# Performance work log

Measured on AMD Instinct MI355X. Metric: run time of the kernel, lower is better.

## Reference

```python
import jax, jax.numpy as jnp
import numpy as np

DIM = 512
HEADS = 8
DIM_HEAD = 64
DIM_INNER = HEADS * DIM_HEAD
SCALE = DIM_HEAD ** -0.5


def setup_inputs() -> dict:
    key = jax.random.key(0)
    ks = jax.random.split(key, 8)
    b, n = 2, 1024
    x = jax.random.normal(ks[0], (b, n, DIM), dtype=jnp.float32)
    w = lambda k, i, o: jax.random.normal(k, (i, o), dtype=jnp.float32) * 0.02
    return {
        'x': x,
        'w_q_u': w(ks[1], DIM, DIM_INNER),
        'w_k_u': w(ks[2], DIM, DIM_INNER),
        'w_v_u': w(ks[3], DIM, DIM_INNER),
        'w_q_c': w(ks[4], DIM, DIM_INNER),
        'w_k_c': w(ks[5], DIM, DIM_INNER),
        'w_v_c': w(ks[6], DIM, DIM_INNER),
        'w_out': w(ks[7], DIM_INNER, DIM),
    }


def reference(x, w_q_u, w_k_u, w_v_u, w_q_c, w_k_c, w_v_c, w_out):
    b, n, _ = x.shape

    def proj(w):  # [b,n,dim] -> [b,h,n,d]
        return (x @ w).reshape(b, n, HEADS, DIM_HEAD).transpose(0, 2, 1, 3)

    q_u, k_u, v_u = proj(w_q_u), proj(w_k_u), proj(w_v_u)
    q_c, k_c, v_c = proj(w_q_c), proj(w_k_c), proj(w_v_c)

    idx = jnp.arange(n)
    causal = idx[:, None] >= idx[None, :]  # tril ones (binary causal mask)

    # term1 = (q_c @ v_u^T) * scale, zeroed above diagonal
    term1 = jnp.einsum('bhid,bhjd->bhij', q_c, v_u) * SCALE
    term1 = term1 * causal.astype(term1.dtype)

    # sigmoid term: (q_u @ k_u^T)*scale with lookahead mask tril(-inf, diag=0)
    logits_u = jnp.einsum('bhid,bhjd->bhij', q_u, k_u) * SCALE
    sig = jax.nn.sigmoid(jnp.where(causal, -jnp.inf, logits_u))

    # S_u[i,k] = sum_j term1[i,j] * sig[k,j]
    S_u = jnp.einsum('bhij,bhkj->bhik', term1, sig)

    # S_c: causal-masked QK
    S_c = jnp.einsum('bhid,bhjd->bhij', q_c, k_c) * SCALE
    S_c = jnp.where(causal, S_c, -jnp.inf)

    final_scores = S_c - jax.nn.silu(S_u)
    attn = jax.nn.softmax(final_scores, axis=-1)
    out = jnp.einsum('bhij,bhjd->bhid', attn, v_c)  # [b,h,n,d]
    out = out.transpose(0, 2, 1, 3).reshape(b, n, DIM_INNER)
    return out @ w_out
```

## Files before the change

kernel.cpp:

```cpp
#include <hip/hip_runtime.h>
#include <math.h>


typedef __bf16 bf16x8 __attribute__((ext_vector_type(8)));
typedef float f32x4 __attribute__((ext_vector_type(4)));

#define SCALE 0.125f

#define GLL(g, l) __builtin_amdgcn_global_load_lds(                         \
    (const __attribute__((address_space(1))) void*)(g),                     \
    (__attribute__((address_space(3))) void*)(l), 16, 0, 0)

__device__ __forceinline__ unsigned short f2bf(float f){
  unsigned int x = __builtin_bit_cast(unsigned int, f);
  unsigned int r = (x + 0x7fffu + ((x >> 16) & 1u)) >> 16;
  return (unsigned short)r;
}
__device__ __forceinline__ float bf2f(unsigned short u){
  unsigned int x = ((unsigned int)u) << 16;
  return __builtin_bit_cast(float, x);
}
__device__ __forceinline__ f32x4 mfma16(bf16x8 a, bf16x8 b, f32x4 c){
  return __builtin_amdgcn_mfma_f32_16x16x32_bf16(a, b, c, 0, 0, 0);
}
__device__ __forceinline__ bf16x8 ld8(const unsigned short* p){
  return *(const bf16x8*)p;
}

__device__ const unsigned char QK_CUM[16] =
  {0,1,2,4,6,9,12,16,20,25,30,36,42,49,56,64};

__device__ const unsigned char FL_RB[40] =
  {15,14,13,12,15,11,14,10,13, 9,12, 8,15,11, 7,14,10, 6,13, 9,
    5,12, 8, 4,15,11, 7, 3,14,10, 6, 2,13, 9, 5, 1,12, 8, 4, 0};
__device__ const unsigned char FL_G[40] =
  { 0, 0, 0, 0, 1, 0, 1, 0, 1, 0, 1, 0, 2, 1, 0, 2, 1, 0, 2, 1,
    0, 2, 1, 0, 3, 2, 1, 0, 3, 2, 1, 0, 3, 2, 1, 0, 3, 2, 1, 0};

__global__ __launch_bounds__(256) void k_prep(
    const float* __restrict__ x,
    const float* __restrict__ w0, const float* __restrict__ w1,
    const float* __restrict__ w2, const float* __restrict__ w3,
    const float* __restrict__ w4, const float* __restrict__ w5,
    const float* __restrict__ w6,
    unsigned short* __restrict__ xb, unsigned short* __restrict__ wT){
  int t = threadIdx.x;
  if (blockIdx.x < 576){
    for (int i = blockIdx.x * 256 + t; i < 262144; i += 576 * 256){
      float4 v = ((const float4*)x)[i];
      ushort4 o; o.x = f2bf(v.x); o.y = f2bf(v.y); o.z = f2bf(v.z); o.w = f2bf(v.w);
      ((ushort4*)xb)[i] = o;
    }
    return;
  }
  __shared__ float lds[64 * 65];
  int bx = blockIdx.x - 576;
  int mat = bx >> 6, tile = bx & 63, tr = tile >> 3, tc = tile & 7;
  int k0 = tr * 64, c0 = tc * 64;
  const float* src;
  switch (mat){
    case 0: src = w0; break; case 1: src = w1; break; case 2: src = w2; break;
    case 3: src = w3; break; case 4: src = w4; break; case 5: src = w5; break;
    default: src = w6; break;
  }
#pragma unroll
  for (int i = 0; i < 4; ++i){
    int r = (t >> 4) + i * 16, c4 = (t & 15) * 4;
    float4 v = *(const float4*)(src + (size_t)(k0 + r) * 512 + c0 + c4);
    lds[r * 65 + c4 + 0] = v.x; lds[r * 65 + c4 + 1] = v.y;
    lds[r * 65 + c4 + 2] = v.z; lds[r * 65 + c4 + 3] = v.w;
  }
  __syncthreads();
  unsigned short* dst = wT + (size_t)mat * 262144;
#pragma unroll
  for (int i = 0; i < 4; ++i){
    int oc = (t >> 4) + i * 16;
    int kq = (t & 15) * 4;
    ushort4 o;
    o.x = f2bf(lds[(kq + 0) * 65 + oc]);
    o.y = f2bf(lds[(kq + 1) * 65 + oc]);
    o.z = f2bf(lds[(kq + 2) * 65 + oc]);
    o.w = f2bf(lds[(kq + 3) * 65 + oc]);
    *(ushort4*)(dst + (size_t)(c0 + oc) * 512 + k0 + kq) = o;
  }
}

__global__ __launch_bounds__(256) void k_proj(
    const unsigned short* __restrict__ xb, const unsigned short* __restrict__ wT,
    unsigned short* __restrict__ P){
  __shared__ __align__(16) unsigned short sA[2 * 2 * 64 * 32];
  __shared__ __align__(16) unsigned short sB[2 * 2 * 128 * 32];
  int t = threadIdx.x, lane = t & 63, l16 = lane & 15, quad = lane >> 4;
  int w = t >> 6, wm = w >> 1, wn = w & 1;
  int bx = blockIdx.x;
  int mt = bx / 24, nt = bx - mt * 24;
  int M0 = mt * 64, N0 = nt * 128;
  int matb = N0 >> 9;
  int nin = N0 & 511;
  int srow = (lane >> 2), scol = (lane & 3) * 8;
  const unsigned short* gA = xb + (size_t)(M0 + w*16 + srow) * 512 + scol;
  const unsigned short* gB = wT + (size_t)matb * 262144
                               + (size_t)(nin + w*32 + srow) * 512 + scol;
  unsigned short* lA = sA + (w*16) * 32;
  unsigned short* lB = sB + (w*32) * 32;
  f32x4 acc[4][2] = {};
#define STAGE_PROJ(buf, k0) do {                                   \
    GLL(gA + (k0),               lA + (buf)*4096);                 \
    GLL(gB + (k0),               lB + (buf)*8192);                 \
    GLL(gB + (k0) + 16*512,      lB + (buf)*8192 + 16*32);         \
    GLL(gA + (k0) + 32,          lA + (buf)*4096 + 2048);          \
    GLL(gB + (k0) + 32,          lB + (buf)*8192 + 4096);          \
    GLL(gB + (k0) + 32 + 16*512, lB + (buf)*8192 + 4096 + 16*32);  \
  } while(0)
  STAGE_PROJ(0, 0);
  for (int it = 0; it < 8; ++it){
    if (it < 7){
      STAGE_PROJ((it+1) & 1, (it+1)*64);
      asm volatile("s_waitcnt vmcnt(6)" ::: "memory");
    } else {
      asm volatile("s_waitcnt vmcnt(0)" ::: "memory");
    }
    __builtin_amdgcn_s_barrier();
    int b = it & 1;
#pragma unroll
    for (int h = 0; h < 2; ++h){
      bf16x8 aw[4], ax[2];
#pragma unroll
      for (int fi = 0; fi < 4; ++fi)
        aw[fi] = *(const bf16x8*)(sB + b*8192 + h*4096 + (wn*64 + fi*16 + l16) * 32 + quad * 8);
#pragma unroll
      for (int mi = 0; mi < 2; ++mi)
        ax[mi] = *(const bf16x8*)(sA + b*4096 + h*2048 + (wm*32 + mi*16 + l16) * 32 + quad * 8);
#pragma unroll
      for (int fi = 0; fi < 4; ++fi)
#pragma unroll
        for (int mi = 0; mi < 2; ++mi)
          acc[fi][mi] = mfma16(aw[fi], ax[mi], acc[fi][mi]);
    }
    __builtin_amdgcn_s_barrier();
  }
#undef STAGE_PROJ
#pragma unroll
  for (int fi = 0; fi < 4; ++fi)
#pragma unroll
    for (int mi = 0; mi < 2; ++mi){
      int row = M0 + wm*32 + mi*16 + l16;
      int b_ = row >> 10, n_ = row & 1023;
      int c0 = N0 + wn*64 + fi*16 + quad*4;
      int h = (c0 & 511) >> 6, d = c0 & 63;
      int bh = b_*8 + h;
      ushort4 o;
      o.x = f2bf(acc[fi][mi][0]); o.y = f2bf(acc[fi][mi][1]);
      o.z = f2bf(acc[fi][mi][2]); o.w = f2bf(acc[fi][mi][3]);
      *(ushort4*)(P + (size_t)(matb*16 + bh) * 65536 + (size_t)n_ * 64 + d) = o;
    }
}

__global__ __launch_bounds__(256) void k_qk_vct(
    const unsigned short* __restrict__ P,
    unsigned short* __restrict__ term1, unsigned short* __restrict__ sig,
    unsigned short* __restrict__ vcT){
  int t = threadIdx.x;
  if (blockIdx.x < 256){
    __shared__ unsigned short lds[64 * 72];
    int bh = blockIdx.x >> 4, nt = blockIdx.x & 15;
    int N0 = nt * 64;
    const unsigned short* src = P + (size_t)(5*16 + bh) * 65536 + (size_t)N0 * 64;
#pragma unroll
    for (int i2 = 0; i2 < 2; ++i2){
      int id = i2 * 256 + t;
      int r = id >> 3, c8 = (id & 7) * 8;
      ushort4 v0 = *(const ushort4*)(src + r * 64 + c8);
      ushort4 v1 = *(const ushort4*)(src + r * 64 + c8 + 4);
      *(ushort4*)(lds + r * 72 + c8) = v0;
      *(ushort4*)(lds + r * 72 + c8 + 4) = v1;
    }
    __syncthreads();
    unsigned short* dst = vcT + (size_t)bh * 65536;
#pragma unroll
    for (int i2 = 0; i2 < 2; ++i2){
      int id = i2 * 256 + t;
      int dd = id >> 3, n8 = (id & 7) * 8;
      ushort4 a, b;
      a.x = lds[(n8+0)*72 + dd]; a.y = lds[(n8+1)*72 + dd];
      a.z = lds[(n8+2)*72 + dd]; a.w = lds[(n8+3)*72 + dd];
      b.x = lds[(n8+4)*72 + dd]; b.y = lds[(n8+5)*72 + dd];
      b.z = lds[(n8+6)*72 + dd]; b.w = lds[(n8+7)*72 + dd];
      *(ushort4*)(dst + (size_t)dd * 1024 + N0 + n8) = a;
      *(ushort4*)(dst + (size_t)dd * 1024 + N0 + n8 + 4) = b;
    }
    return;
  }
  __shared__ unsigned short sA[2 * 64 * 32], sB[2 * 128 * 32];
  int id = blockIdx.x - 256;
  int bh = id & 15, tt = id >> 4;
  int mat = (tt >= 72);
  int tl = mat ? tt - 72 : tt;
  int rb = 15;
  while (QK_CUM[rb] > tl) --rb;
  int ct = tl - QK_CUM[rb];
  int R0, C0;
  const unsigned short *Asrc, *Bsrc;
  if (!mat){ R0 = rb * 64;        C0 = ct * 128;
             Asrc = P + (size_t)(3*16 + bh) * 65536;
             Bsrc = P + (size_t)(2*16 + bh) * 65536; }
  else     { R0 = (15 - rb) * 64; C0 = (7 - ct) * 128;
             Asrc = P + (size_t)(0*16 + bh) * 65536;
             Bsrc = P + (size_t)(1*16 + bh) * 65536; }
  int lane = t & 63, l16 = lane & 15, quad = lane >> 4;
  int w = t >> 6, wm = w >> 1, wn = w & 1;
  int srow = lane >> 2, scol = (lane & 3) * 8;
  const unsigned short* gA = Asrc + (size_t)(R0 + w*16 + srow) * 64 + scol;
  const unsigned short* gB = Bsrc + (size_t)(C0 + w*32 + srow) * 64 + scol;
  unsigned short* lA0 = sA + (w*16) * 32;
  unsigned short* lB0 = sB + (w*32) * 32;
  unsigned short* lA1 = lA0 + 64 * 32;
  unsigned short* lB1 = lB0 + 128 * 32;
  f32x4 acc[4][2] = {};
  GLL(gA,              lA0);
  GLL(gB,              lB0);
  GLL(gB + 16*64,      lB0 + 16*32);
  GLL(gA + 32,         lA1);
  GLL(gB + 32,         lB1);
  GLL(gB + 32 + 16*64, lB1 + 16*32);
  __syncthreads();
#pragma unroll
  for (int h = 0; h < 2; ++h){
    bf16x8 af[2], bfr[4];
#pragma unroll
    for (int mi = 0; mi < 2; ++mi)
      af[mi] = *(const bf16x8*)(sA + h*2048 + (wm*32 + mi*16 + l16) * 32 + quad * 8);
#pragma unroll
    for (int fi = 0; fi < 4; ++fi)
      bfr[fi] = *(const bf16x8*)(sB + h*4096 + (wn*64 + fi*16 + l16) * 32 + quad * 8);
#pragma unroll
    for (int fi = 0; fi < 4; ++fi)
#pragma unroll
      for (int mi = 0; mi < 2; ++mi)
        acc[fi][mi] = mfma16(bfr[fi], af[mi], acc[fi][mi]);
  }
  unsigned short* out = (mat ? sig : term1) + (size_t)bh * 1048576;
#pragma unroll
  for (int fi = 0; fi < 4; ++fi)
#pragma unroll
    for (int mi = 0; mi < 2; ++mi){
      int row = R0 + wm*32 + mi*16 + l16;
      int c0 = C0 + wn*64 + fi*16 + quad*4;
      ushort4 o;
#pragma unroll
      for (int r = 0; r < 4; ++r){
        int col = c0 + r;
        float v = acc[fi][mi][r] * SCALE;
        unsigned short res;
        if (!mat) res = (col <= row) ? f2bf(v) : (unsigned short)0;
        else      res = (col >  row) ? f2bf(1.f / (1.f + expf(-v))) : (unsigned short)0;
        ((unsigned short*)&o)[r] = res;
      }
      *(ushort4*)(out + (size_t)row * 1024 + c0) = o;
    }
}

__global__ __launch_bounds__(256) void k_flash(
    const unsigned short* __restrict__ P,
    const unsigned short* __restrict__ term1,
    const unsigned short* __restrict__ sig,
    const unsigned short* __restrict__ vcT,
    float* __restrict__ Opart, float* __restrict__ MS,
    unsigned short* __restrict__ O2){
  __shared__ __align__(16) unsigned short sA[2 * 64 * 32];
  __shared__ __align__(16) unsigned short sB[2 * 128 * 32];
  __shared__ __align__(16) unsigned short probs[64 * 136];
  __shared__ float wpm[2][64], wps[2][64];
  __shared__ float alpha_s[64], mrun_s[64], srun_s[64];
  int t = threadIdx.x;
  int bh = blockIdx.x & 15, q = blockIdx.x >> 4;
  int rb = FL_RB[q], g = FL_G[q];
  int T = (rb >> 1) + 1, G = (T + 1) >> 1;
  int ct0 = 2 * g, ctN = min(ct0 + 2, T);
  int R0 = rb * 64;
  size_t sbase = (size_t)bh * 1048576;
  int lane = t & 63, l16 = lane & 15, quad = lane >> 4, w = t >> 6;
  int wm = w >> 1, wn = w & 1;
  int srow = lane >> 2, scol = (lane & 3) * 8;
  unsigned short* lA0 = sA + (w*16) * 32;
  unsigned short* lB0 = sB + (w*32) * 32;
  unsigned short* lA1 = lA0 + 2048;
  unsigned short* lB1 = lB0 + 4096;
  const unsigned short* Qc = P + (size_t)(3*16 + bh) * 65536;
  const unsigned short* Kc = P + (size_t)(4*16 + bh) * 65536;
  const unsigned short* Vt = vcT + (size_t)bh * 65536;
  if (t < 64){ mrun_s[t] = -INFINITY; srun_s[t] = 0.f; }
  bf16x8 aq[2][2];
#pragma unroll
  for (int mi = 0; mi < 2; ++mi)
#pragma unroll
    for (int kk = 0; kk < 2; ++kk)
      aq[mi][kk] = ld8(Qc + (size_t)(R0 + wm*32 + mi*16 + l16) * 64 + kk*32 + quad*8);
  f32x4 acc_o[4] = {};
  const unsigned short* gA = term1 + sbase + (size_t)(R0 + w*16 + srow) * 1024 + scol;
  const unsigned short* gBs = sig  + sbase;

  for (int ct = ct0; ct < ctN; ++ct){
    int C0 = ct * 128;
    int n_it = rb + 1 - 2*ct;
    const unsigned short* gB = gBs + (size_t)(C0 + w*32 + srow) * 1024 + scol;
    f32x4 acc_u[4][2] = {};
    for (int it = 0; it < n_it; ++it){
      int j0 = C0 + it * 64;
      GLL(gA + j0,              lA0);
      GLL(gB + j0,              lB0);
      GLL(gB + j0 + 16*1024,    lB0 + 16*32);
      GLL(gA + j0 + 32,           lA1);
      GLL(gB + j0 + 32,           lB1);
      GLL(gB + j0 + 32 + 16*1024, lB1 + 16*32);
      __syncthreads();
#pragma unroll
      for (int h = 0; h < 2; ++h){
        bf16x8 af[2], bfr[4];
#pragma unroll
        for (int mi = 0; mi < 2; ++mi)
          af[mi] = *(const bf16x8*)(sA + h*2048 + (wm*32 + mi*16 + l16) * 32 + quad * 8);
#pragma unroll
        for (int fi = 0; fi < 4; ++fi)
          bfr[fi] = *(const bf16x8*)(sB + h*4096 + (wn*64 + fi*16 + l16) * 32 + quad * 8);
#pragma unroll
        for (int fi = 0; fi < 4; ++fi)
#pragma unroll
          for (int mi = 0; mi < 2; ++mi)
            acc_u[fi][mi] = mfma16(bfr[fi], af[mi], acc_u[fi][mi]);
      }
      __syncthreads();
    }
    f32x4 acc_c[4][2] = {};
#pragma unroll
    for (int kk = 0; kk < 2; ++kk){
      bf16x8 bfr[4];
#pragma unroll
      for (int fi = 0; fi < 4; ++fi)
        bfr[fi] = ld8(Kc + (size_t)(C0 + wn*64 + fi*16 + l16) * 64 + kk*32 + quad*8);
#pragma unroll
      for (int fi = 0; fi < 4; ++fi)
#pragma unroll
        for (int mi = 0; mi < 2; ++mi)
          acc_c[fi][mi] = mfma16(bfr[fi], aq[mi][kk], acc_c[fi][mi]);
    }
    float pm0 = -INFINITY, pm1 = -INFINITY;
#pragma unroll
    for (int fi = 0; fi < 4; ++fi)
#pragma unroll
      for (int mi = 0; mi < 2; ++mi){
        int row = R0 + wm*32 + mi*16 + l16;
        int c0 = C0 + wn*64 + fi*16 + quad*4;
#pragma unroll
        for (int r = 0; r < 4; ++r){
          float su = acc_u[fi][mi][r];
          float s = acc_c[fi][mi][r] * SCALE - su / (1.f + expf(-su));
          if (c0 + r > row) s = -INFINITY;
          acc_u[fi][mi][r] = s;
          if (mi) pm1 = fmaxf(pm1, s); else pm0 = fmaxf(pm0, s);
        }
      }
    pm0 = fmaxf(pm0, __shfl_xor(pm0, 16)); pm0 = fmaxf(pm0, __shfl_xor(pm0, 32));
    pm1 = fmaxf(pm1, __shfl_xor(pm1, 16)); pm1 = fmaxf(pm1, __shfl_xor(pm1, 32));
    if (quad == 0){
      wpm[wn][wm*32 + l16]      = pm0;
      wpm[wn][wm*32 + 16 + l16] = pm1;
    }
    __syncthreads();
    if (t < 64){
      float pmax = fmaxf(wpm[0][t], wpm[1][t]);
      float mo = mrun_s[t], mn = fmaxf(mo, pmax);
      alpha_s[t] = expf(mo - mn);
      mrun_s[t] = mn;
    }
    __syncthreads();
    float mr0 = mrun_s[wm*32 + l16], mr1 = mrun_s[wm*32 + 16 + l16];
    float ps0 = 0.f, ps1 = 0.f;
#pragma unroll
    for (int fi = 0; fi < 4; ++fi)
#pragma unroll
      for (int mi = 0; mi < 2; ++mi){
        ushort4 o;
#pragma unroll
        for (int r = 0; r < 4; ++r){
          float p = expf(acc_u[fi][mi][r] - (mi ? mr1 : mr0));
          if (mi) ps1 += p; else ps0 += p;
          ((unsigned short*)&o)[r] = f2bf(p);
        }
        *(ushort4*)(probs + (wm*32 + mi*16 + l16) * 136 + wn*64 + fi*16 + quad*4) = o;
      }
    ps0 += __shfl_xor(ps0, 16); ps0 += __shfl_xor(ps0, 32);
    ps1 += __shfl_xor(ps1, 16); ps1 += __shfl_xor(ps1, 32);
    if (quad == 0){
      wps[wn][wm*32 + l16]      = ps0;
      wps[wn][wm*32 + 16 + l16] = ps1;
    }
    __syncthreads();
    if (t < 64) srun_s[t] = srun_s[t] * alpha_s[t] + wps[0][t] + wps[1][t];
    float al[4];
#pragma unroll
    for (int r = 0; r < 4; ++r) al[r] = alpha_s[16*w + quad*4 + r];
#pragma unroll
    for (int fi = 0; fi < 4; ++fi)
#pragma unroll
      for (int r = 0; r < 4; ++r) acc_o[fi][r] *= al[r];
    const unsigned short* pr = probs + (16*w + l16) * 136 + quad * 8;
#pragma unroll
    for (int k0 = 0; k0 < 4; ++k0){
      bf16x8 a = *(const bf16x8*)(pr + k0*32);
#pragma unroll
      for (int fi = 0; fi < 4; ++fi){
        bf16x8 b = ld8(Vt + (size_t)(fi*16 + l16) * 1024 + C0 + k0*32 + quad*8);
        acc_o[fi] = mfma16(a, b, acc_o[fi]);
      }
    }
  }
  __syncthreads();
  float* red = (float*)probs;
#pragma unroll
  for (int fi = 0; fi < 4; ++fi)
#pragma unroll
    for (int r = 0; r < 4; ++r)
      red[(16*w + quad*4 + r) * 64 + fi*16 + l16] = acc_o[fi][r];
  __syncthreads();
  int b_ = bh >> 3, h_ = bh & 7;
  if (G == 1){
#pragma unroll
    for (int pass = 0; pass < 4; ++pass){
      int e = pass * 1024 + t * 4;
      int row = e >> 6, col = e & 63;
      float inv = 1.f / srun_s[row];
      float4 v = *(const float4*)(red + e);
      ushort4 o;
      o.x = f2bf(v.x * inv); o.y = f2bf(v.y * inv);
      o.z = f2bf(v.z * inv); o.w = f2bf(v.w * inv);
      *(ushort4*)(O2 + (size_t)(b_*1024 + R0 + row) * 512 + h_*64 + col) = o;
    }
  } else {
    int slot = bh * 64 + rb * 4 + g;
#pragma unroll
    for (int pass = 0; pass < 4; ++pass){
      int e = pass * 1024 + t * 4;
      *(float4*)(Opart + (size_t)slot * 4096 + e) = *(const float4*)(red + e);
    }
    if (t < 64){
      MS[(size_t)slot * 128 + t*2]     = mrun_s[t];
      MS[(size_t)slot * 128 + t*2 + 1] = srun_s[t];
    }
  }
}

__global__ __launch_bounds__(256) void k_comb(
    const float* __restrict__ Opart, const float* __restrict__ MS,
    unsigned short* __restrict__ O2){
  int t = threadIdx.x;
  int bh = blockIdx.x & 15, rb = 4 + (blockIdx.x >> 4);
  int T = (rb >> 1) + 1, G = (T + 1) >> 1;
  int r = t >> 2, cb = (t & 3) * 16;
  int base = bh * 64 + rb * 4;
  float m = -INFINITY;
#pragma unroll
  for (int g2 = 0; g2 < 4; ++g2)
    if (g2 < G) m = fmaxf(m, MS[(size_t)(base + g2) * 128 + r*2]);
  float wg0 = 0.f, wg1 = 0.f, wg2 = 0.f, wg3 = 0.f, den = 0.f;
  if (0 < G){ wg0 = expf(MS[(size_t)(base+0)*128 + r*2] - m); den += MS[(size_t)(base+0)*128 + r*2 + 1] * wg0; }
  if (1 < G){ wg1 = expf(MS[(size_t)(base+1)*128 + r*2] - m); den += MS[(size_t)(base+1)*128 + r*2 + 1] * wg1; }
  if (2 < G){ wg2 = expf(MS[(size_t)(base+2)*128 + r*2] - m); den += MS[(size_t)(base+2)*128 + r*2 + 1] * wg2; }
  if (3 < G){ wg3 = expf(MS[(size_t)(base+3)*128 + r*2] - m); den += MS[(size_t)(base+3)*128 + r*2 + 1] * wg3; }
  float inv = 1.f / den;
  int b_ = bh >> 3, h_ = bh & 7;
#pragma unroll
  for (int c4 = 0; c4 < 4; ++c4){
    float ax = 0.f, ay = 0.f, az = 0.f, aw = 0.f;
#pragma unroll
    for (int g2 = 0; g2 < 4; ++g2){
      if (g2 < G){
        float wgv = (g2 == 0) ? wg0 : (g2 == 1) ? wg1 : (g2 == 2) ? wg2 : wg3;
        float4 v = *(const float4*)(Opart + (size_t)(base + g2) * 4096 + r*64 + cb + c4*4);
        ax += v.x * wgv; ay += v.y * wgv; az += v.z * wgv; aw += v.w * wgv;
      }
    }
    ushort4 o;
    o.x = f2bf(ax * inv); o.y = f2bf(ay * inv);
    o.z = f2bf(az * inv); o.w = f2bf(aw * inv);
    *(ushort4*)(O2 + (size_t)(b_*1024 + rb*64 + r) * 512 + h_*64 + cb + c4*4) = o;
  }
}

__global__ __launch_bounds__(256) void k_out(
    const unsigned short* __restrict__ O2, const unsigned short* __restrict__ woT,
    float* __restrict__ out){
  __shared__ float red[4][1024];
  int t = threadIdx.x, lane = t & 63, l16 = lane & 15, quad = lane >> 4, w = t >> 6;
  int mt = blockIdx.x >> 3, nt = blockIdx.x & 7;
  int m0 = mt * 16, n0 = nt * 64;
  int r_ = m0 + l16;
  f32x4 acc[4] = {};
#pragma unroll
  for (int s = 0; s < 4; ++s){
    int kk = w * 128 + s * 32 + quad * 8;
    bf16x8 a = ld8(O2 + (size_t)r_ * 512 + kk);
#pragma unroll
    for (int fi = 0; fi < 4; ++fi){
      bf16x8 b = ld8(woT + (size_t)(n0 + fi*16 + l16) * 512 + kk);
      acc[fi] = mfma16(a, b, acc[fi]);
    }
  }
#pragma unroll
  for (int fi = 0; fi < 4; ++fi)
#pragma unroll
    for (int r = 0; r < 4; ++r)
      red[w][(quad*4 + r) * 64 + fi*16 + l16] = acc[fi][r];
  __syncthreads();
  float4 a0 = ((const float4*)red[0])[t];
  float4 a1 = ((const float4*)red[1])[t];
  float4 a2 = ((const float4*)red[2])[t];
  float4 a3 = ((const float4*)red[3])[t];
  float4 o;
  o.x = a0.x + a1.x + a2.x + a3.x;
  o.y = a0.y + a1.y + a2.y + a3.y;
  o.z = a0.z + a1.z + a2.z + a3.z;
  o.w = a0.w + a1.w + a2.w + a3.w;
  int e = t * 4, row = e >> 6, col = e & 63;
  *(float4*)(out + (size_t)(m0 + row) * 512 + n0 + col) = o;
}

extern "C" void kernel_launch(void* const* d_in, const int* in_sizes, int n_in,
                              void* d_out, int out_size, void* d_ws, size_t ws_size,
                              hipStream_t stream){
  const float* x = (const float*)d_in[0];
  float* out = (float*)d_out;
  unsigned short* ws = (unsigned short*)d_ws;

  unsigned short* wT    = ws;
  unsigned short* xb    = wT    + (size_t)7  * 262144;
  unsigned short* P     = xb    + (size_t)1048576;
  unsigned short* vcT   = P     + (size_t)96 * 65536;
  unsigned short* term1 = vcT   + (size_t)16 * 65536;
  unsigned short* sig   = term1 + (size_t)16 * 1048576;
  unsigned short* O2    = sig   + (size_t)16 * 1048576;
  unsigned short* fwsp  = O2    + (size_t)16 * 65536;
  float* Opart = (float*)fwsp;
  float* MS    = Opart + (size_t)1024 * 4096;

  k_prep<<<1024, 256, 0, stream>>>(
      x,
      (const float*)d_in[1], (const float*)d_in[2], (const float*)d_in[3],
      (const float*)d_in[4], (const float*)d_in[5], (const float*)d_in[6],
      (const float*)d_in[7], xb, wT);
  k_proj<<<768, 256, 0, stream>>>(xb, wT, P);
  k_qk_vct<<<2560, 256, 0, stream>>>(P, term1, sig, vcT);
  k_flash<<<640, 256, 0, stream>>>(P, term1, sig, vcT, Opart, MS, O2);
  k_comb<<<192, 256, 0, stream>>>(Opart, MS, O2);
  k_out<<<1024, 256, 0, stream>>>(O2, wT + (size_t)6 * 262144, out);
}
```

Measured before the change: 165.7 us.

## Replace LDS-staged tiles with direct global fragment loads in QK and flash kernels

Removes the shared-memory staging (global_load_lds plus barriers) in both the projection-score kernel and the S_u accumulation loop of the flash kernel, loading MFMA operand fragments directly from global memory into registers. The intent is to drop the per-iteration __syncthreads and LDS round trips and free LDS for higher occupancy. In exchange, each wave re-reads data that warps previously shared, which adds global/L2 traffic and makes the loop more exposed to memory latency.

Result: slower. 204.3 us (+23.3%).

```diff
diff --git a/kernel.cpp b/kernel.cpp
--- a/kernel.cpp
+++ b/kernel.cpp
@@ -191,7 +191,6 @@
     }
     return;
   }
-  __shared__ unsigned short sA[2 * 64 * 32], sB[2 * 128 * 32];
   int id = blockIdx.x - 256;
   int bh = id & 15, tt = id >> 4;
   int mat = (tt >= 72);
@@ -209,30 +208,16 @@
              Bsrc = P + (size_t)(1*16 + bh) * 65536; }
   int lane = t & 63, l16 = lane & 15, quad = lane >> 4;
   int w = t >> 6, wm = w >> 1, wn = w & 1;
-  int srow = lane >> 2, scol = (lane & 3) * 8;
-  const unsigned short* gA = Asrc + (size_t)(R0 + w*16 + srow) * 64 + scol;
-  const unsigned short* gB = Bsrc + (size_t)(C0 + w*32 + srow) * 64 + scol;
-  unsigned short* lA0 = sA + (w*16) * 32;
-  unsigned short* lB0 = sB + (w*32) * 32;
-  unsigned short* lA1 = lA0 + 64 * 32;
-  unsigned short* lB1 = lB0 + 128 * 32;
   f32x4 acc[4][2] = {};
-  GLL(gA,              lA0);
-  GLL(gB,              lB0);
-  GLL(gB + 16*64,      lB0 + 16*32);
-  GLL(gA + 32,         lA1);
-  GLL(gB + 32,         lB1);
-  GLL(gB + 32 + 16*64, lB1 + 16*32);
-  __syncthreads();
-#pragma unroll
-  for (int h = 0; h < 2; ++h){
+#pragma unroll
+  for (int kk = 0; kk < 64; kk += 32){
     bf16x8 af[2], bfr[4];
 #pragma unroll
     for (int mi = 0; mi < 2; ++mi)
-      af[mi] = *(const bf16x8*)(sA + h*2048 + (wm*32 + mi*16 + l16) * 32 + quad * 8);
+      af[mi] = ld8(Asrc + (size_t)(R0 + wm*32 + mi*16 + l16) * 64 + kk + quad*8);
 #pragma unroll
     for (int fi = 0; fi < 4; ++fi)
-      bfr[fi] = *(const bf16x8*)(sB + h*4096 + (wn*64 + fi*16 + l16) * 32 + quad * 8);
+      bfr[fi] = ld8(Bsrc + (size_t)(C0 + wn*64 + fi*16 + l16) * 64 + kk + quad*8);
 #pragma unroll
     for (int fi = 0; fi < 4; ++fi)
 #pragma unroll
@@ -267,8 +252,6 @@
     const unsigned short* __restrict__ vcT,
     float* __restrict__ Opart, float* __restrict__ MS,
     unsigned short* __restrict__ O2){
-  __shared__ __align__(16) unsigned short sA[2 * 64 * 32];
-  __shared__ __align__(16) unsigned short sB[2 * 128 * 32];
   __shared__ __align__(16) unsigned short probs[64 * 136];
   __shared__ float wpm[2][64], wps[2][64];
   __shared__ float alpha_s[64], mrun_s[64], srun_s[64];
@@ -281,11 +264,6 @@
   size_t sbase = (size_t)bh * 1048576;
   int lane = t & 63, l16 = lane & 15, quad = lane >> 4, w = t >> 6;
   int wm = w >> 1, wn = w & 1;
-  int srow = lane >> 2, scol = (lane & 3) * 8;
-  unsigned short* lA0 = sA + (w*16) * 32;
-  unsigned short* lB0 = sB + (w*32) * 32;
-  unsigned short* lA1 = lA0 + 2048;
-  unsigned short* lB1 = lB0 + 4096;
   const unsigned short* Qc = P + (size_t)(3*16 + bh) * 65536;
   const unsigned short* Kc = P + (size_t)(4*16 + bh) * 65536;
   const unsigned short* Vt = vcT + (size_t)bh * 65536;
@@ -297,39 +275,34 @@
     for (int kk = 0; kk < 2; ++kk)
       aq[mi][kk] = ld8(Qc + (size_t)(R0 + wm*32 + mi*16 + l16) * 64 + kk*32 + quad*8);
   f32x4 acc_o[4] = {};
-  const unsigned short* gA = term1 + sbase + (size_t)(R0 + w*16 + srow) * 1024 + scol;
-  const unsigned short* gBs = sig  + sbase;
+  const unsigned short* arow0 = term1 + sbase + (size_t)(R0 + wm*32 + l16) * 1024 + quad*8;
+  const unsigned short* arow1 = arow0 + (size_t)16 * 1024;
+  const unsigned short* gBs = sig + sbase;
 
   for (int ct = ct0; ct < ctN; ++ct){
     int C0 = ct * 128;
-    int n_it = rb + 1 - 2*ct;
-    const unsigned short* gB = gBs + (size_t)(C0 + w*32 + srow) * 1024 + scol;
+    int jEnd = R0 + 64;
+    const unsigned short* brow0 = gBs + (size_t)(C0 + wn*64 + l16) * 1024 + quad*8;
+    const unsigned short* brow1 = brow0 + (size_t)16 * 1024;
+    const unsigned short* brow2 = brow0 + (size_t)32 * 1024;
+    const unsigned short* brow3 = brow0 + (size_t)48 * 1024;
     f32x4 acc_u[4][2] = {};
-    for (int it = 0; it < n_it; ++it){
-      int j0 = C0 + it * 64;
-      GLL(gA + j0,              lA0);
-      GLL(gB + j0,              lB0);
-      GLL(gB + j0 + 16*1024,    lB0 + 16*32);
-      GLL(gA + j0 + 32,           lA1);
-      GLL(gB + j0 + 32,           lB1);
-      GLL(gB + j0 + 32 + 16*1024, lB1 + 16*32);
-      __syncthreads();
-#pragma unroll
-      for (int h = 0; h < 2; ++h){
-        bf16x8 af[2], bfr[4];
-#pragma unroll
-        for (int mi = 0; mi < 2; ++mi)
-          af[mi] = *(const bf16x8*)(sA + h*2048 + (wm*32 + mi*16 + l16) * 32 + quad * 8);
-#pragma unroll
-        for (int fi = 0; fi < 4; ++fi)
-          bfr[fi] = *(const bf16x8*)(sB + h*4096 + (wn*64 + fi*16 + l16) * 32 + quad * 8);
-#pragma unroll
-        for (int fi = 0; fi < 4; ++fi)
-#pragma unroll
-          for (int mi = 0; mi < 2; ++mi)
-            acc_u[fi][mi] = mfma16(bfr[fi], af[mi], acc_u[fi][mi]);
-      }
-      __syncthreads();
+#pragma unroll 2
+    for (int j = C0; j < jEnd; j += 32){
+      bf16x8 af0 = ld8(arow0 + j);
+      bf16x8 af1 = ld8(arow1 + j);
+      bf16x8 b0 = ld8(brow0 + j);
+      bf16x8 b1 = ld8(brow1 + j);
+      bf16x8 b2 = ld8(brow2 + j);
+      bf16x8 b3 = ld8(brow3 + j);
+      acc_u[0][0] = mfma16(b0, af0, acc_u[0][0]);
+      acc_u[0][1] = mfma16(b0, af1, acc_u[0][1]);
+      acc_u[1][0] = mfma16(b1, af0, acc_u[1][0]);
+      acc_u[1][1] = mfma16(b1, af1, acc_u[1][1]);
+      acc_u[2][0] = mfma16(b2, af0, acc_u[2][0]);
+      acc_u[2][1] = mfma16(b2, af1, acc_u[2][1]);
+      acc_u[3][0] = mfma16(b3, af0, acc_u[3][0]);
+      acc_u[3][1] = mfma16(b3, af1, acc_u[3][1]);
     }
     f32x4 acc_c[4][2] = {};
 #pragma unroll
```

## Split flash kernel into one block per (row-block, column-tile) with split-K combine

Applied to the files above, without the earlier changes.

Each flash block now handles exactly one 128-column tile for a 64-row block instead of looping over up to two tiles with an online softmax. Partial outputs, maxima and sums for all 72 tiles per head are written out, and the combine kernel merges up to 8 partials for every row block, including the short ones. The goal is more parallelism and better load balance, with a heavy-first schedule table, plus a smaller LDS footprint from aliasing the buffers. The cost is extra partial-output traffic and a combine pass that now runs for all row blocks.

New measurement: 168.8 us. No clear change (+1.9%).

```diff
diff --git a/kernel.cpp b/kernel.cpp
--- a/kernel.cpp
+++ b/kernel.cpp
@@ -30,12 +30,18 @@
 __device__ const unsigned char QK_CUM[16] =
   {0,1,2,4,6,9,12,16,20,25,30,36,42,49,56,64};
 
-__device__ const unsigned char FL_RB[40] =
-  {15,14,13,12,15,11,14,10,13, 9,12, 8,15,11, 7,14,10, 6,13, 9,
-    5,12, 8, 4,15,11, 7, 3,14,10, 6, 2,13, 9, 5, 1,12, 8, 4, 0};
-__device__ const unsigned char FL_G[40] =
-  { 0, 0, 0, 0, 1, 0, 1, 0, 1, 0, 1, 0, 2, 1, 0, 2, 1, 0, 2, 1,
-    0, 2, 1, 0, 3, 2, 1, 0, 3, 2, 1, 0, 3, 2, 1, 0, 3, 2, 1, 0};
+__device__ const unsigned char SC_RB[72] =
+  {15,14,11,13,15,10,12,14,15,14,13,12,15,13,11, 9,
+   12, 8, 6,15,13,11, 9, 7,15,13,14,10,14,12,10, 8,
+    9, 3,14,12,10, 8, 6, 4,15,13,11, 7,11, 9, 7, 5,
+   13,10, 8,11, 9, 6, 4, 2,15,14,12, 5, 7, 5, 3, 1,
+   14,12,10, 8, 6, 4, 2, 0};
+__device__ const unsigned char SC_CT[72] =
+  { 1, 1, 0, 1, 2, 0, 1, 2, 0, 0, 0, 0, 3, 2, 1, 0,
+    3, 1, 0, 4, 3, 2, 1, 0, 5, 4, 4, 2, 3, 2, 1, 0,
+    3, 0, 5, 4, 3, 2, 1, 0, 6, 5, 4, 2, 3, 2, 1, 0,
+    6, 4, 3, 5, 4, 2, 1, 0, 7, 6, 5, 1, 3, 2, 1, 0,
+    7, 6, 5, 4, 3, 2, 1, 0};
 
 __global__ __launch_bounds__(256) void k_prep(
     const float* __restrict__ x,
@@ -265,19 +271,18 @@
     const unsigned short* __restrict__ term1,
     const unsigned short* __restrict__ sig,
     const unsigned short* __restrict__ vcT,
-    float* __restrict__ Opart, float* __restrict__ MS,
-    unsigned short* __restrict__ O2){
-  __shared__ __align__(16) unsigned short sA[2 * 64 * 32];
-  __shared__ __align__(16) unsigned short sB[2 * 128 * 32];
-  __shared__ __align__(16) unsigned short probs[64 * 136];
+    float* __restrict__ Opart, float* __restrict__ MS){
+  __shared__ __align__(16) unsigned short smem[2*64*32 + 2*128*32];
+  unsigned short* sA = smem;
+  unsigned short* sB = smem + 4096;
+  unsigned short* probs = smem;
+  float* red = (float*)smem;
   __shared__ float wpm[2][64], wps[2][64];
-  __shared__ float alpha_s[64], mrun_s[64], srun_s[64];
   int t = threadIdx.x;
-  int bh = blockIdx.x & 15, q = blockIdx.x >> 4;
-  int rb = FL_RB[q], g = FL_G[q];
-  int T = (rb >> 1) + 1, G = (T + 1) >> 1;
-  int ct0 = 2 * g, ctN = min(ct0 + 2, T);
-  int R0 = rb * 64;
+  int bh = blockIdx.x & 15, tt = blockIdx.x >> 4;
+  int rb = SC_RB[tt], ct = SC_CT[tt];
+  int R0 = rb * 64, C0 = ct * 128;
+  int n_it = rb + 1 - 2*ct;
   size_t sbase = (size_t)bh * 1048576;
   int lane = t & 63, l16 = lane & 15, quad = lane >> 4, w = t >> 6;
   int wm = w >> 1, wn = w & 1;
@@ -289,164 +294,124 @@
   const unsigned short* Qc = P + (size_t)(3*16 + bh) * 65536;
   const unsigned short* Kc = P + (size_t)(4*16 + bh) * 65536;
   const unsigned short* Vt = vcT + (size_t)bh * 65536;
-  if (t < 64){ mrun_s[t] = -INFINITY; srun_s[t] = 0.f; }
-  bf16x8 aq[2][2];
-#pragma unroll
-  for (int mi = 0; mi < 2; ++mi)
-#pragma unroll
-    for (int kk = 0; kk < 2; ++kk)
-      aq[mi][kk] = ld8(Qc + (size_t)(R0 + wm*32 + mi*16 + l16) * 64 + kk*32 + quad*8);
+  const unsigned short* gA = term1 + sbase + (size_t)(R0 + w*16 + srow) * 1024 + scol;
+  const unsigned short* gB = sig   + sbase + (size_t)(C0 + w*32 + srow) * 1024 + scol;
+  f32x4 acc_u[4][2] = {};
+  for (int it = 0; it < n_it; ++it){
+    int j0 = C0 + it * 64;
+    GLL(gA + j0,                lA0);
+    GLL(gB + j0,                lB0);
+    GLL(gB + j0 + 16*1024,      lB0 + 16*32);
+    GLL(gA + j0 + 32,           lA1);
+    GLL(gB + j0 + 32,           lB1);
+    GLL(gB + j0 + 32 + 16*1024, lB1 + 16*32);
+    __syncthreads();
+#pragma unroll
+    for (int h = 0; h < 2; ++h){
+      bf16x8 af[2], bfr[4];
+#pragma unroll
+      for (int mi = 0; mi < 2; ++mi)
+        af[mi] = *(const bf16x8*)(sA + h*2048 + (wm*32 + mi*16 + l16) * 32 + quad * 8);
+#pragma unroll
+      for (int fi = 0; fi < 4; ++fi)
+        bfr[fi] = *(const bf16x8*)(sB + h*4096 + (wn*64 + fi*16 + l16) * 32 + quad * 8);
+#pragma unroll
+      for (int fi = 0; fi < 4; ++fi)
+#pragma unroll
+        for (int mi = 0; mi < 2; ++mi)
+          acc_u[fi][mi] = mfma16(bfr[fi], af[mi], acc_u[fi][mi]);
+    }
+    __syncthreads();
+  }
+  f32x4 acc_c[4][2] = {};
+#pragma unroll
+  for (int kk = 0; kk < 2; ++kk){
+    bf16x8 aqk[2], bfr[4];
+#pragma unroll
+    for (int mi = 0; mi < 2; ++mi)
+      aqk[mi] = ld8(Qc + (size_t)(R0 + wm*32 + mi*16 + l16) * 64 + kk*32 + quad*8);
+#pragma unroll
+    for (int fi = 0; fi < 4; ++fi)
+      bfr[fi] = ld8(Kc + (size_t)(C0 + wn*64 + fi*16 + l16) * 64 + kk*32 + quad*8);
+#pragma unroll
+    for (int fi = 0; fi < 4; ++fi)
+#pragma unroll
+      for (int mi = 0; mi < 2; ++mi)
+        acc_c[fi][mi] = mfma16(bfr[fi], aqk[mi], acc_c[fi][mi]);
+  }
+  float pm0 = -INFINITY, pm1 = -INFINITY;
+#pragma unroll
+  for (int fi = 0; fi < 4; ++fi)
+#pragma unroll
+    for (int mi = 0; mi < 2; ++mi){
+      int row = R0 + wm*32 + mi*16 + l16;
+      int c0 = C0 + wn*64 + fi*16 + quad*4;
+#pragma unroll
+      for (int r = 0; r < 4; ++r){
+        float su = acc_u[fi][mi][r];
+        float s = acc_c[fi][mi][r] * SCALE - su / (1.f + expf(-su));
+        if (c0 + r > row) s = -INFINITY;
+        acc_u[fi][mi][r] = s;
+        if (mi) pm1 = fmaxf(pm1, s); else pm0 = fmaxf(pm0, s);
+      }
+    }
+  pm0 = fmaxf(pm0, __shfl_xor(pm0, 16)); pm0 = fmaxf(pm0, __shfl_xor(pm0, 32));
+  pm1 = fmaxf(pm1, __shfl_xor(pm1, 16)); pm1 = fmaxf(pm1, __shfl_xor(pm1, 32));
+  if (quad == 0){
+    wpm[wn][wm*32 + l16]      = pm0;
+    wpm[wn][wm*32 + 16 + l16] = pm1;
+  }
+  __syncthreads();
+  float mr0 = fmaxf(wpm[0][wm*32 + l16],      wpm[1][wm*32 + l16]);
+  float mr1 = fmaxf(wpm[0][wm*32 + 16 + l16], wpm[1][wm*32 + 16 + l16]);
+  float ps0 = 0.f, ps1 = 0.f;
+#pragma unroll
+  for (int fi = 0; fi < 4; ++fi)
+#pragma unroll
+    for (int mi = 0; mi < 2; ++mi){
+      ushort4 o;
+#pragma unroll
+      for (int r = 0; r < 4; ++r){
+        float p = expf(acc_u[fi][mi][r] - (mi ? mr1 : mr0));
+        if (mi) ps1 += p; else ps0 += p;
+        ((unsigned short*)&o)[r] = f2bf(p);
+      }
+      *(ushort4*)(probs + (wm*32 + mi*16 + l16) * 136 + wn*64 + fi*16 + quad*4) = o;
+    }
+  ps0 += __shfl_xor(ps0, 16); ps0 += __shfl_xor(ps0, 32);
+  ps1 += __shfl_xor(ps1, 16); ps1 += __shfl_xor(ps1, 32);
+  if (quad == 0){
+    wps[wn][wm*32 + l16]      = ps0;
+    wps[wn][wm*32 + 16 + l16] = ps1;
+  }
+  __syncthreads();
   f32x4 acc_o[4] = {};
-  const unsigned short* gA = term1 + sbase + (size_t)(R0 + w*16 + srow) * 1024 + scol;
-  const unsigned short* gBs = sig  + sbase;
-
-  for (int ct = ct0; ct < ctN; ++ct){
-    int C0 = ct * 128;
-    int n_it = rb + 1 - 2*ct;
-    const unsigned short* gB = gBs + (size_t)(C0 + w*32 + srow) * 1024 + scol;
-    f32x4 acc_u[4][2] = {};
-    for (int it = 0; it < n_it; ++it){
-      int j0 = C0 + it * 64;
-      GLL(gA + j0,              lA0);
-      GLL(gB + j0,              lB0);
-      GLL(gB + j0 + 16*1024,    lB0 + 16*32);
-      GLL(gA + j0 + 32,           lA1);
-      GLL(gB + j0 + 32,           lB1);
-      GLL(gB + j0 + 32 + 16*1024, lB1 + 16*32);
-      __syncthreads();
-#pragma unroll
-      for (int h = 0; h < 2; ++h){
-        bf16x8 af[2], bfr[4];
-#pragma unroll
-        for (int mi = 0; mi < 2; ++mi)
-          af[mi] = *(const bf16x8*)(sA + h*2048 + (wm*32 + mi*16 + l16) * 32 + quad * 8);
-#pragma unroll
-        for (int fi = 0; fi < 4; ++fi)
-          bfr[fi] = *(const bf16x8*)(sB + h*4096 + (wn*64 + fi*16 + l16) * 32 + quad * 8);
-#pragma unroll
-        for (int fi = 0; fi < 4; ++fi)
-#pragma unroll
-          for (int mi = 0; mi < 2; ++mi)
-            acc_u[fi][mi] = mfma16(bfr[fi], af[mi], acc_u[fi][mi]);
-      }
-      __syncthreads();
-    }
-    f32x4 acc_c[4][2] = {};
-#pragma unroll
-    for (int kk = 0; kk < 2; ++kk){
-      bf16x8 bfr[4];
-#pragma unroll
-      for (int fi = 0; fi < 4; ++fi)
-        bfr[fi] = ld8(Kc + (size_t)(C0 + wn*64 + fi*16 + l16) * 64 + kk*32 + quad*8);
-#pragma unroll
-      for (int fi = 0; fi < 4; ++fi)
-#pragma unroll
-        for (int mi = 0; mi < 2; ++mi)
-          acc_c[fi][mi] = mfma16(bfr[fi], aq[mi][kk], acc_c[fi][mi]);
-    }
-    float pm0 = -INFINITY, pm1 = -INFINITY;
-#pragma unroll
-    for (int fi = 0; fi < 4; ++fi)
-#pragma unroll
-      for (int mi = 0; mi < 2; ++mi){
-        int row = R0 + wm*32 + mi*16 + l16;
-        int c0 = C0 + wn*64 + fi*16 + quad*4;
-#pragma unroll
-        for (int r = 0; r < 4; ++r){
-          float su = acc_u[fi][mi][r];
-          float s = acc_c[fi][mi][r] * SCALE - su / (1.f + expf(-su));
-          if (c0 + r > row) s = -INFINITY;
-          acc_u[fi][mi][r] = s;
-          if (mi) pm1 = fmaxf(pm1, s); else pm0 = fmaxf(pm0, s);
-        }
-      }
-    pm0 = fmaxf(pm0, __shfl_xor(pm0, 16)); pm0 = fmaxf(pm0, __shfl_xor(pm0, 32));
-    pm1 = fmaxf(pm1, __shfl_xor(pm1, 16)); pm1 = fmaxf(pm1, __shfl_xor(pm1, 32));
-    if (quad == 0){
-      wpm[wn][wm*32 + l16]      = pm0;
-      wpm[wn][wm*32 + 16 + l16] = pm1;
-    }
-    __syncthreads();
-    if (t < 64){
-      float pmax = fmaxf(wpm[0][t], wpm[1][t]);
-      float mo = mrun_s[t], mn = fmaxf(mo, pmax);
-      alpha_s[t] = expf(mo - mn);
-      mrun_s[t] = mn;
-    }
-    __syncthreads();
-    float mr0 = mrun_s[wm*32 + l16], mr1 = mrun_s[wm*32 + 16 + l16];
-    float ps0 = 0.f, ps1 = 0.f;
-#pragma unroll
-    for (int fi = 0; fi < 4; ++fi)
-#pragma unroll
-      for (int mi = 0; mi < 2; ++mi){
-        ushort4 o;
-#pragma unroll
-        for (int r = 0; r < 4; ++r){
-          float p = expf(acc_u[fi][mi][r] - (mi ? mr1 : mr0));
-          if (mi) ps1 += p; else ps0 += p;
-          ((unsigned short*)&o)[r] = f2bf(p);
-        }
-        *(ushort4*)(probs + (wm*32 + mi*16 + l16) * 136 + wn*64 + fi*16 + quad*4) = o;
-      }
-    ps0 += __shfl_xor(ps0, 16); ps0 += __shfl_xor(ps0, 32);
-    ps1 += __shfl_xor(ps1, 16); ps1 += __shfl_xor(ps1, 32);
-    if (quad == 0){
-      wps[wn][wm*32 + l16]      = ps0;
-      wps[wn][wm*32 + 16 + l16] = ps1;
-    }
-    __syncthreads();
-    if (t < 64) srun_s[t] = srun_s[t] * alpha_s[t] + wps[0][t] + wps[1][t];
-    float al[4];
-#pragma unroll
-    for (int r = 0; r < 4; ++r) al[r] = alpha_s[16*w + quad*4 + r];
-#pragma unroll
-    for (int fi = 0; fi < 4; ++fi)
-#pragma unroll
-      for (int r = 0; r < 4; ++r) acc_o[fi][r] *= al[r];
-    const unsigned short* pr = probs + (16*w + l16) * 136 + quad * 8;
-#pragma unroll
-    for (int k0 = 0; k0 < 4; ++k0){
-      bf16x8 a = *(const bf16x8*)(pr + k0*32);
-#pragma unroll
-      for (int fi = 0; fi < 4; ++fi){
-        bf16x8 b = ld8(Vt + (size_t)(fi*16 + l16) * 1024 + C0 + k0*32 + quad*8);
-        acc_o[fi] = mfma16(a, b, acc_o[fi]);
-      }
-    }
-  }
-  __syncthreads();
-  float* red = (float*)probs;
+  const unsigned short* pr = probs + (16*w + l16) * 136 + quad * 8;
+#pragma unroll
+  for (int k0 = 0; k0 < 4; ++k0){
+    bf16x8 a = *(const bf16x8*)(pr + k0*32);
+#pragma unroll
+    for (int fi = 0; fi < 4; ++fi){
+      bf16x8 b = ld8(Vt + (size_t)(fi*16 + l16) * 1024 + C0 + k0*32 + quad*8);
+      acc_o[fi] = mfma16(a, b, acc_o[fi]);
+    }
+  }
+  __syncthreads();
 #pragma unroll
   for (int fi = 0; fi < 4; ++fi)
 #pragma unroll
     for (int r = 0; r < 4; ++r)
       red[(16*w + quad*4 + r) * 64 + fi*16 + l16] = acc_o[fi][r];
   __syncthreads();
-  int b_ = bh >> 3, h_ = bh & 7;
-  if (G == 1){
-#pragma unroll
-    for (int pass = 0; pass < 4; ++pass){
-      int e = pass * 1024 + t * 4;
-      int row = e >> 6, col = e & 63;
-      float inv = 1.f / srun_s[row];
-      float4 v = *(const float4*)(red + e);
-      ushort4 o;
-      o.x = f2bf(v.x * inv); o.y = f2bf(v.y * inv);
-      o.z = f2bf(v.z * inv); o.w = f2bf(v.w * inv);
-      *(ushort4*)(O2 + (size_t)(b_*1024 + R0 + row) * 512 + h_*64 + col) = o;
-    }
-  } else {
-    int slot = bh * 64 + rb * 4 + g;
-#pragma unroll
-    for (int pass = 0; pass < 4; ++pass){
-      int e = pass * 1024 + t * 4;
-      *(float4*)(Opart + (size_t)slot * 4096 + e) = *(const float4*)(red + e);
-    }
-    if (t < 64){
-      MS[(size_t)slot * 128 + t*2]     = mrun_s[t];
-      MS[(size_t)slot * 128 + t*2 + 1] = srun_s[t];
-    }
+  int slot = bh * 72 + QK_CUM[rb] + ct;
+#pragma unroll
+  for (int pass = 0; pass < 4; ++pass){
+    int e = pass * 1024 + t * 4;
+    *(float4*)(Opart + (size_t)slot * 4096 + e) = *(const float4*)(red + e);
+  }
+  if (t < 64){
+    MS[(size_t)slot * 128 + t*2]     = fmaxf(wpm[0][t], wpm[1][t]);
+    MS[(size_t)slot * 128 + t*2 + 1] = wps[0][t] + wps[1][t];
   }
 }
 
@@ -454,30 +419,33 @@
     const float* __restrict__ Opart, const float* __restrict__ MS,
     unsigned short* __restrict__ O2){
   int t = threadIdx.x;
-  int bh = blockIdx.x & 15, rb = 4 + (blockIdx.x >> 4);
-  int T = (rb >> 1) + 1, G = (T + 1) >> 1;
+  int bh = blockIdx.x & 15, rb = blockIdx.x >> 4;
+  int G = (rb >> 1) + 1;
   int r = t >> 2, cb = (t & 3) * 16;
-  int base = bh * 64 + rb * 4;
+  int base = bh * 72 + QK_CUM[rb];
   float m = -INFINITY;
 #pragma unroll
-  for (int g2 = 0; g2 < 4; ++g2)
+  for (int g2 = 0; g2 < 8; ++g2)
     if (g2 < G) m = fmaxf(m, MS[(size_t)(base + g2) * 128 + r*2]);
-  float wg0 = 0.f, wg1 = 0.f, wg2 = 0.f, wg3 = 0.f, den = 0.f;
-  if (0 < G){ wg0 = expf(MS[(size_t)(base+0)*128 + r*2] - m); den += MS[(size_t)(base+0)*128 + r*2 + 1] * wg0; }
-  if (1 < G){ wg1 = expf(MS[(size_t)(base+1)*128 + r*2] - m); den += MS[(size_t)(base+1)*128 + r*2 + 1] * wg1; }
-  if (2 < G){ wg2 = expf(MS[(size_t)(base+2)*128 + r*2] - m); den += MS[(size_t)(base+2)*128 + r*2 + 1] * wg2; }
-  if (3 < G){ wg3 = expf(MS[(size_t)(base+3)*128 + r*2] - m); den += MS[(size_t)(base+3)*128 + r*2 + 1] * wg3; }
+  float wg[8]; float den = 0.f;
+#pragma unroll
+  for (int g2 = 0; g2 < 8; ++g2){
+    if (g2 < G){
+      wg[g2] = expf(MS[(size_t)(base + g2) * 128 + r*2] - m);
+      den += MS[(size_t)(base + g2) * 128 + r*2 + 1] * wg[g2];
+    } else wg[g2] = 0.f;
+  }
   float inv = 1.f / den;
   int b_ = bh >> 3, h_ = bh & 7;
 #pragma unroll
   for (int c4 = 0; c4 < 4; ++c4){
     float ax = 0.f, ay = 0.f, az = 0.f, aw = 0.f;
 #pragma unroll
-    for (int g2 = 0; g2 < 4; ++g2){
+    for (int g2 = 0; g2 < 8; ++g2){
       if (g2 < G){
-        float wgv = (g2 == 0) ? wg0 : (g2 == 1) ? wg1 : (g2 == 2) ? wg2 : wg3;
         float4 v = *(const float4*)(Opart + (size_t)(base + g2) * 4096 + r*64 + cb + c4*4);
-        ax += v.x * wgv; ay += v.y * wgv; az += v.z * wgv; aw += v.w * wgv;
+        ax += v.x * wg[g2]; ay += v.y * wg[g2];
+        az += v.z * wg[g2]; aw += v.w * wg[g2];
       }
     }
     ushort4 o;
@@ -541,7 +509,7 @@
   unsigned short* O2    = sig   + (size_t)16 * 1048576;
   unsigned short* fwsp  = O2    + (size_t)16 * 65536;
   float* Opart = (float*)fwsp;
-  float* MS    = Opart + (size_t)1024 * 4096;
+  float* MS    = Opart + (size_t)1152 * 4096;
 
   k_prep<<<1024, 256, 0, stream>>>(
       x,
@@ -550,7 +518,7 @@
       (const float*)d_in[7], xb, wT);
   k_proj<<<768, 256, 0, stream>>>(xb, wT, P);
   k_qk_vct<<<2560, 256, 0, stream>>>(P, term1, sig, vcT);
-  k_flash<<<640, 256, 0, stream>>>(P, term1, sig, vcT, Opart, MS, O2);
-  k_comb<<<192, 256, 0, stream>>>(Opart, MS, O2);
+  k_flash<<<1152, 256, 0, stream>>>(P, term1, sig, vcT, Opart, MS);
+  k_comb<<<256, 256, 0, stream>>>(Opart, MS, O2);
   k_out<<<1024, 256, 0, stream>>>(O2, wT + (size_t)6 * 262144, out);
 }
```
